# Kernel optimization log

Hardware: AMD Instinct MI355X
Metric: run time of the kernel (lower is better)

## Reference

```python
import jax, jax.numpy as jnp
import numpy as np

N, E, G = 100000, 1600000, 64
IN, H, OUT = 128, 64, 16  # hidden/2 = 32
SLOPE = 0.01


def setup_inputs() -> dict:
    key = jax.random.key(0)
    ks = jax.random.split(key, 7)
    features = jax.random.normal(ks[0], (N, IN), dtype=jnp.float32)
    src = jax.random.randint(ks[1], (E,), 0, N)
    dst = jax.random.randint(ks[2], (E,), 0, N)
    graph_ids = jnp.sort(jax.random.randint(ks[3], (N,), 0, G))
    # kaiming-uniform-ish fan_in init, bias=False everywhere
    W1 = jax.random.uniform(ks[4], (IN, H), jnp.float32, -1.0, 1.0) * np.sqrt(3.0 / IN)
    W2 = jax.random.uniform(ks[5], (H, H // 2), jnp.float32, -1.0, 1.0) * np.sqrt(3.0 / H)
    Wc = jax.random.uniform(ks[6], (H // 2, OUT), jnp.float32, -1.0, 1.0) * np.sqrt(3.0 / (H // 2))
    return {"features": features, "src": src, "dst": dst, "graph_ids": graph_ids,
            "W1": W1, "W2": W2, "Wc": Wc}


def _graph_conv(x, W, src, dst, n):
    # DGL GraphConv, norm='both', bias=False:
    # out = D_in^{-1/2} A (D_out^{-1/2} x) W   (degrees clamped to >= 1)
    ones = jnp.ones(src.shape[0], dtype=x.dtype)
    outdeg = jnp.clip(jax.ops.segment_sum(ones, src, num_segments=n), 1.0)
    indeg = jnp.clip(jax.ops.segment_sum(ones, dst, num_segments=n), 1.0)
    h = (x * jax.lax.rsqrt(outdeg)[:, None]) @ W  # project first (in_dim > out_dim)
    m = jax.ops.segment_sum(h[src], dst, num_segments=n)  # sparse aggregation
    return m * jax.lax.rsqrt(indeg)[:, None]


def reference(features, src, dst, graph_ids, W1, W2, Wc):
    h = jax.nn.leaky_relu(_graph_conv(features, W1, src, dst, N), SLOPE)
    h = jax.nn.leaky_relu(_graph_conv(h, W2, src, dst, N), SLOPE)
    # dropout is identity at inference
    sums = jax.ops.segment_sum(h, graph_ids, num_segments=G)
    cnts = jnp.clip(jax.ops.segment_sum(jnp.ones((N,), h.dtype), graph_ids, num_segments=G), 1.0)
    mean = sums / cnts[:, None]  # dgl.mean_nodes
    return mean @ Wc  # [G, OUT]
```

## Files before the change

kernel.cpp:

```cpp
#include <hip/hip_runtime.h>

#define NN 100000
#define NE 1600000
#define NG 64
#define D_IN 128
#define D_H 64
#define D_H2 32
#define D_OUT 16
#define SLOPE 0.01f
#define REC 48

#define BSH 9
#define NBK 196
#define NCB 250
#define CHE (NE / NCB)
#define CNT_M (2 * NBK * NCB)
#define CNT_R 98048

typedef _Float16 half2v __attribute__((ext_vector_type(2)));
typedef _Float16 h8 __attribute__((ext_vector_type(8)));
typedef float f32x4 __attribute__((ext_vector_type(4)));

__global__ __launch_bounds__(256) void p1_count(const int* __restrict__ src,
                                                const int* __restrict__ dst,
                                                int* __restrict__ cnt) {
  __shared__ int hD[NBK], hS[NBK];
  int b = blockIdx.x, t = threadIdx.x;
  if (b == 0 && t < CNT_R - CNT_M) cnt[CNT_M + t] = 0;
  for (int i = t; i < NBK; i += 256) { hD[i] = 0; hS[i] = 0; }
  __syncthreads();
  const int4* s4 = (const int4*)(src + b * CHE);
  const int4* d4 = (const int4*)(dst + b * CHE);
  for (int i = t; i < CHE / 4; i += 256) {
    int4 s = s4[i], d = d4[i];
    atomicAdd(&hD[d.x >> BSH], 1); atomicAdd(&hD[d.y >> BSH], 1);
    atomicAdd(&hD[d.z >> BSH], 1); atomicAdd(&hD[d.w >> BSH], 1);
    atomicAdd(&hS[s.x >> BSH], 1); atomicAdd(&hS[s.y >> BSH], 1);
    atomicAdd(&hS[s.z >> BSH], 1); atomicAdd(&hS[s.w >> BSH], 1);
  }
  __syncthreads();
  for (int i = t; i < NBK; i += 256) {
    cnt[i * NCB + b] = hD[i];
    cnt[(NBK + i) * NCB + b] = hS[i];
  }
}

__global__ __launch_bounds__(256) void s1_reduce(const int* __restrict__ cnt,
                                                 int* __restrict__ part) {
  __shared__ int red[256];
  int b = blockIdx.x, t = threadIdx.x;
  red[t] = cnt[b * 256 + t];
  __syncthreads();
  for (int off = 128; off > 0; off >>= 1) {
    if (t < off) red[t] += red[t + off];
    __syncthreads();
  }
  if (t == 0) part[b] = red[0];
}

__global__ __launch_bounds__(512) void s2_scan(int* __restrict__ part) {
  __shared__ int a[512], b2[512];
  int t = threadIdx.x;
  const int M = CNT_R / 256;
  int v = (t < M) ? part[t] : 0;
  a[t] = v;
  __syncthreads();
  int* cur = a; int* nxt = b2;
  for (int off = 1; off < 512; off <<= 1) {
    int x = cur[t];
    if (t >= off) x += cur[t - off];
    nxt[t] = x;
    __syncthreads();
    int* tmp = cur; cur = nxt; nxt = tmp;
  }
  if (t < M) part[t] = cur[t] - v;
}

__global__ __launch_bounds__(256) void s3_apply(int* __restrict__ cnt,
                                                const int* __restrict__ part) {
  __shared__ int wsum[4];
  int b = blockIdx.x, t = threadIdx.x;
  int gid = b * 256 + t;
  int v0 = cnt[gid];
  int lane = t & 63, w = t >> 6;
  int v = v0;
  for (int off = 1; off < 64; off <<= 1) {
    int u = __shfl_up(v, off);
    if (lane >= off) v += u;
  }
  if (lane == 63) wsum[w] = v;
  __syncthreads();
  int woff = 0;
  for (int i = 0; i < w; ++i) woff += wsum[i];
  cnt[gid] = part[b] + woff + (v - v0);
}

__global__ __launch_bounds__(256) void p2_scatter(const int* __restrict__ src,
                                                  const int* __restrict__ dst,
                                                  const int* __restrict__ cnt,
                                                  unsigned* __restrict__ pk,
                                                  unsigned short* __restrict__ srcs16) {
  __shared__ int cD[NBK], cS[NBK];
  int b = blockIdx.x, t = threadIdx.x;
  for (int i = t; i < NBK; i += 256) {
    cD[i] = cnt[i * NCB + b];
    cS[i] = cnt[(NBK + i) * NCB + b] - NE;
  }
  __syncthreads();
  const int4* s4 = (const int4*)(src + b * CHE);
  const int4* d4 = (const int4*)(dst + b * CHE);
  for (int i = t; i < CHE / 4; i += 256) {
    int4 s = s4[i], d = d4[i];
#pragma unroll
    for (int j = 0; j < 4; ++j) {
      int ss = (j == 0) ? s.x : (j == 1) ? s.y : (j == 2) ? s.z : s.w;
      int dd = (j == 0) ? d.x : (j == 1) ? d.y : (j == 2) ? d.z : d.w;
      int pd = atomicAdd(&cD[dd >> BSH], 1);
      pk[pd] = ((unsigned)(dd & 511) << 17) | (unsigned)ss;
      int ps = atomicAdd(&cS[ss >> BSH], 1);
      srcs16[ps] = (unsigned short)(ss & 511);
    }
  }
}

__global__ __launch_bounds__(256) void p3_build(const unsigned* __restrict__ pk,
                                                const unsigned short* __restrict__ srcs16,
                                                const int* __restrict__ cnt,
                                                int* __restrict__ adj,
                                                int* __restrict__ indeg,
                                                int* __restrict__ outdeg) {
  __shared__ int hh[512];
  int bb = blockIdx.x, t = threadIdx.x;
  for (int i = t; i < 512; i += 256) hh[i] = 0;
  __syncthreads();
  if (bb < NBK) {
    int k = bb;
    int n0 = k << BSH;
    int lo = cnt[k * NCB];
    int hi = cnt[(k + 1) * NCB];
    for (int i = lo + t; i < hi; i += 256) {
      unsigned v = pk[i];
      int local = v >> 17;
      int pos = atomicAdd(&hh[local], 1);
      if (pos < REC) adj[(size_t)(n0 + local) * REC + pos] = (int)(v & 0x1FFFF);
    }
    __syncthreads();
    for (int i = t; i < 512; i += 256) {
      int n = n0 + i;
      if (n < NN) {
        int dg = hh[i];
        indeg[n] = dg;
        int d = min(dg, REC);
        int dr = min((d + 15) & ~15, REC);
        for (int j = d; j < dr; ++j) adj[(size_t)n * REC + j] = NN;
      }
    }
  } else {
    int k = bb - NBK;
    int lo = cnt[(NBK + k) * NCB] - NE;
    int hi = ((k == NBK - 1) ? 2 * NE : cnt[(NBK + k + 1) * NCB]) - NE;
    for (int i = lo + t; i < hi; i += 256) atomicAdd(&hh[srcs16[i]], 1);
    __syncthreads();
    int n0 = k << BSH;
    for (int i = t; i < 512; i += 256) {
      int n = n0 + i;
      if (n < NN) outdeg[n] = hh[i];
    }
  }
}

__global__ __launch_bounds__(256) void k_mm1f(const float* __restrict__ X,
                                              const float* __restrict__ W,
                                              const int* __restrict__ odeg,
                                              _Float16* __restrict__ Y) {
  __shared__ _Float16 Wt[64][136];
  int t = threadIdx.x;
  if (blockIdx.x == 0 && t < 64) Y[(size_t)NN * 64 + t] = (_Float16)0.f;
  for (int i = t; i < 128 * 64; i += 256) {
    int k = i >> 6, f = i & 63;
    Wt[f][k] = (_Float16)W[i];
  }
  __syncthreads();
  int lane = t & 63, w = t >> 6;
  int m = lane & 15, q = lane >> 4;
  h8 bf[4][4];
#pragma unroll
  for (int kc = 0; kc < 4; ++kc)
#pragma unroll
    for (int nt = 0; nt < 4; ++nt)
      bf[kc][nt] = *(const h8*)&Wt[nt * 16 + m][kc * 32 + q * 8];

  for (int tile = blockIdx.x * 4 + w; tile < NN / 16; tile += gridDim.x * 4) {
    int n0 = tile * 16;
    const f32x4* Xr = (const f32x4*)(X + (size_t)(n0 + m) * 128);
    h8 af[4];
#pragma unroll
    for (int kc = 0; kc < 4; ++kc) {
      f32x4 x0 = Xr[kc * 8 + q * 2 + 0];
      f32x4 x1 = Xr[kc * 8 + q * 2 + 1];
      h8 a;
      a[0] = (_Float16)x0.x; a[1] = (_Float16)x0.y;
      a[2] = (_Float16)x0.z; a[3] = (_Float16)x0.w;
      a[4] = (_Float16)x1.x; a[5] = (_Float16)x1.y;
      a[6] = (_Float16)x1.z; a[7] = (_Float16)x1.w;
      af[kc] = a;
    }
    f32x4 acc[4] = {{0,0,0,0},{0,0,0,0},{0,0,0,0},{0,0,0,0}};
#pragma unroll
    for (int kc = 0; kc < 4; ++kc)
#pragma unroll
      for (int nt = 0; nt < 4; ++nt)
        acc[nt] = __builtin_amdgcn_mfma_f32_16x16x32_f16(af[kc], bf[kc][nt], acc[nt], 0, 0, 0);
#pragma unroll
    for (int reg = 0; reg < 4; ++reg) {
      int nn = n0 + q * 4 + reg;
      float sc = rsqrtf((float)max(odeg[nn], 1));
#pragma unroll
      for (int nt = 0; nt < 4; ++nt)
        Y[(size_t)nn * 64 + nt * 16 + m] = (_Float16)(acc[nt][reg] * sc);
    }
  }
}

__global__ __launch_bounds__(256) void k_mm2f(const _Float16* __restrict__ Xh,
                                              const float* __restrict__ W,
                                              const int* __restrict__ odeg,
                                              _Float16* __restrict__ Y) {
  __shared__ _Float16 Wt[32][72];
  int t = threadIdx.x;
  if (blockIdx.x == 0 && t < 32) Y[(size_t)NN * 32 + t] = (_Float16)0.f;
  for (int i = t; i < 64 * 32; i += 256) {
    int k = i >> 5, f = i & 31;
    Wt[f][k] = (_Float16)W[i];
  }
  __syncthreads();
  int lane = t & 63, w = t >> 6;
  int m = lane & 15, q = lane >> 4;
  h8 bf[2][2];
#pragma unroll
  for (int kc = 0; kc < 2; ++kc)
#pragma unroll
    for (int nt = 0; nt < 2; ++nt)
      bf[kc][nt] = *(const h8*)&Wt[nt * 16 + m][kc * 32 + q * 8];

  for (int tile = blockIdx.x * 4 + w; tile < NN / 16; tile += gridDim.x * 4) {
    int n0 = tile * 16;
    const h8* Xr = (const h8*)(Xh + (size_t)(n0 + m) * 64);
    h8 af[2];
#pragma unroll
    for (int kc = 0; kc < 2; ++kc) af[kc] = Xr[kc * 4 + q];
    f32x4 acc[2] = {{0,0,0,0},{0,0,0,0}};
#pragma unroll
    for (int kc = 0; kc < 2; ++kc)
#pragma unroll
      for (int nt = 0; nt < 2; ++nt)
        acc[nt] = __builtin_amdgcn_mfma_f32_16x16x32_f16(af[kc], bf[kc][nt], acc[nt], 0, 0, 0);
#pragma unroll
    for (int reg = 0; reg < 4; ++reg) {
      int nn = n0 + q * 4 + reg;
      float sc = rsqrtf((float)max(odeg[nn], 1));
#pragma unroll
      for (int nt = 0; nt < 2; ++nt)
        Y[(size_t)nn * 32 + nt * 16 + m] = (_Float16)(acc[nt][reg] * sc);
    }
  }
}

__global__ __launch_bounds__(256) void k_agg64(const int* __restrict__ adj,
                                               const int* __restrict__ indeg,
                                               const half2v* __restrict__ H2,
                                               half2v* __restrict__ Y2) {
  int lane = threadIdx.x & 31;
  int node = blockIdx.x * 8 + (threadIdx.x >> 5);
  int deg = indeg[node];
  int groups = (min(deg, REC) + 15) >> 4;
  const int4* c4 = (const int4*)(adj + (size_t)node * REC);
  float sx = 0.f, sy = 0.f;
  for (int g = 0; g < groups; ++g) {
    int4 ca = c4[g * 4 + 0], cb = c4[g * 4 + 1];
    int4 cc = c4[g * 4 + 2], cd = c4[g * 4 + 3];
    half2v v0 = H2[(size_t)ca.x * 32 + lane];
    half2v v1 = H2[(size_t)ca.y * 32 + lane];
    half2v v2 = H2[(size_t)ca.z * 32 + lane];
    half2v v3 = H2[(size_t)ca.w * 32 + lane];
    half2v v4 = H2[(size_t)cb.x * 32 + lane];
    half2v v5 = H2[(size_t)cb.y * 32 + lane];
    half2v v6 = H2[(size_t)cb.z * 32 + lane];
    half2v v7 = H2[(size_t)cb.w * 32 + lane];
    half2v v8 = H2[(size_t)cc.x * 32 + lane];
    half2v v9 = H2[(size_t)cc.y * 32 + lane];
    half2v va = H2[(size_t)cc.z * 32 + lane];
    half2v vb = H2[(size_t)cc.w * 32 + lane];
    half2v vc = H2[(size_t)cd.x * 32 + lane];
    half2v vd = H2[(size_t)cd.y * 32 + lane];
    half2v ve = H2[(size_t)cd.z * 32 + lane];
    half2v vf = H2[(size_t)cd.w * 32 + lane];
    sx += (((float)v0.x + (float)v1.x) + ((float)v2.x + (float)v3.x)) +
          (((float)v4.x + (float)v5.x) + ((float)v6.x + (float)v7.x)) +
          (((float)v8.x + (float)v9.x) + ((float)va.x + (float)vb.x)) +
          (((float)vc.x + (float)vd.x) + ((float)ve.x + (float)vf.x));
    sy += (((float)v0.y + (float)v1.y) + ((float)v2.y + (float)v3.y)) +
          (((float)v4.y + (float)v5.y) + ((float)v6.y + (float)v7.y)) +
          (((float)v8.y + (float)v9.y) + ((float)va.y + (float)vb.y)) +
          (((float)vc.y + (float)vd.y) + ((float)ve.y + (float)vf.y));
  }
  float sc = rsqrtf((float)max(deg, 1));
  sx *= sc; sy *= sc;
  half2v o = {(_Float16)((sx > 0.f) ? sx : SLOPE * sx),
              (_Float16)((sy > 0.f) ? sy : SLOPE * sy)};
  Y2[(size_t)node * 32 + lane] = o;
}

__global__ __launch_bounds__(256) void k_agg32(const int* __restrict__ adj,
                                               const int* __restrict__ indeg,
                                               const half2v* __restrict__ H2,
                                               half2v* __restrict__ Y2) {
  int lane = threadIdx.x & 15;
  int node = blockIdx.x * 16 + (threadIdx.x >> 4);
  int deg = indeg[node];
  int groups = (min(deg, REC) + 15) >> 4;
  const int4* c4 = (const int4*)(adj + (size_t)node * REC);
  float sx = 0.f, sy = 0.f;
  for (int g = 0; g < groups; ++g) {
    int4 ca = c4[g * 4 + 0], cb = c4[g * 4 + 1];
    int4 cc = c4[g * 4 + 2], cd = c4[g * 4 + 3];
    half2v v0 = H2[(size_t)ca.x * 16 + lane];
    half2v v1 = H2[(size_t)ca.y * 16 + lane];
    half2v v2 = H2[(size_t)ca.z * 16 + lane];
    half2v v3 = H2[(size_t)ca.w * 16 + lane];
    half2v v4 = H2[(size_t)cb.x * 16 + lane];
    half2v v5 = H2[(size_t)cb.y * 16 + lane];
    half2v v6 = H2[(size_t)cb.z * 16 + lane];
    half2v v7 = H2[(size_t)cb.w * 16 + lane];
    half2v v8 = H2[(size_t)cc.x * 16 + lane];
    half2v v9 = H2[(size_t)cc.y * 16 + lane];
    half2v va = H2[(size_t)cc.z * 16 + lane];
    half2v vb = H2[(size_t)cc.w * 16 + lane];
    half2v vc = H2[(size_t)cd.x * 16 + lane];
    half2v vd = H2[(size_t)cd.y * 16 + lane];
    half2v ve = H2[(size_t)cd.z * 16 + lane];
    half2v vf = H2[(size_t)cd.w * 16 + lane];
    sx += (((float)v0.x + (float)v1.x) + ((float)v2.x + (float)v3.x)) +
          (((float)v4.x + (float)v5.x) + ((float)v6.x + (float)v7.x)) +
          (((float)v8.x + (float)v9.x) + ((float)va.x + (float)vb.x)) +
          (((float)vc.x + (float)vd.x) + ((float)ve.x + (float)vf.x));
    sy += (((float)v0.y + (float)v1.y) + ((float)v2.y + (float)v3.y)) +
          (((float)v4.y + (float)v5.y) + ((float)v6.y + (float)v7.y)) +
          (((float)v8.y + (float)v9.y) + ((float)va.y + (float)vb.y)) +
          (((float)vc.y + (float)vd.y) + ((float)ve.y + (float)vf.y));
  }
  float sc = rsqrtf((float)max(deg, 1));
  sx *= sc; sy *= sc;
  half2v o = {(_Float16)((sx > 0.f) ? sx : SLOPE * sx),
              (_Float16)((sy > 0.f) ? sy : SLOPE * sy)};
  Y2[(size_t)node * 16 + lane] = o;
}

__global__ void k_bounds(const int* __restrict__ gid, int* __restrict__ bounds) {
  int n = blockIdx.x * 256 + threadIdx.x;
  if (n < NN) {
    int g = gid[n];
    int gp = (n == 0) ? -1 : gid[n - 1];
    for (int j = gp + 1; j <= g; ++j) bounds[j] = n;
    if (n == NN - 1)
      for (int j = g + 1; j <= NG; ++j) bounds[j] = NN;
  }
}

__global__ __launch_bounds__(256) void k_poolout(const half2v* __restrict__ H2,
                                                 const int* __restrict__ bounds,
                                                 const float* __restrict__ Wc,
                                                 float* __restrict__ out) {
  __shared__ float red[16][33];
  __shared__ float mean[D_H2];
  int g = blockIdx.x, t = threadIdx.x;
  int start = bounds[g], end = bounds[g + 1];
  int c2 = t & 15, r = t >> 4;
  float sx = 0.f, sy = 0.f;
  for (int n = start + r; n < end; n += 16) {
    half2v v = H2[(size_t)n * 16 + c2];
    sx += (float)v.x;
    sy += (float)v.y;
  }
  red[r][c2 * 2] = sx;
  red[r][c2 * 2 + 1] = sy;
  __syncthreads();
  if (r < 8) { red[r][c2 * 2] += red[r + 8][c2 * 2]; red[r][c2 * 2 + 1] += red[r + 8][c2 * 2 + 1]; }
  __syncthreads();
  if (r < 4) { red[r][c2 * 2] += red[r + 4][c2 * 2]; red[r][c2 * 2 + 1] += red[r + 4][c2 * 2 + 1]; }
  __syncthreads();
  if (r < 2) { red[r][c2 * 2] += red[r + 2][c2 * 2]; red[r][c2 * 2 + 1] += red[r + 2][c2 * 2 + 1]; }
  __syncthreads();
  if (r == 0) {
    float inv = 1.0f / (float)max(end - start, 1);
    mean[c2 * 2] = (red[0][c2 * 2] + red[1][c2 * 2]) * inv;
    mean[c2 * 2 + 1] = (red[0][c2 * 2 + 1] + red[1][c2 * 2 + 1]) * inv;
  }
  __syncthreads();
  if (t < D_OUT) {
    float acc = 0.f;
#pragma unroll
    for (int cc = 0; cc < D_H2; ++cc) acc += mean[cc] * Wc[cc * D_OUT + t];
    out[g * D_OUT + t] = acc;
  }
}

extern "C" void kernel_launch(void* const* d_in, const int* in_sizes, int n_in,
                              void* d_out, int out_size, void* d_ws, size_t ws_size,
                              hipStream_t stream) {
  const float* X  = (const float*)d_in[0];
  const int*   src = (const int*)d_in[1];
  const int*   dst = (const int*)d_in[2];
  const int*   gid = (const int*)d_in[3];
  const float* W1 = (const float*)d_in[4];
  const float* W2 = (const float*)d_in[5];
  const float* Wc = (const float*)d_in[6];
  float* out = (float*)d_out;

  char* p = (char*)d_ws;
  auto alloc = [&](size_t bytes) {
    char* q = p;
    p += (bytes + 255) & ~(size_t)255;
    return q;
  };
  int*            outdeg = (int*)alloc(NN * 4);
  int*            indeg  = (int*)alloc(NN * 4);
  int*            bounds = (int*)alloc((NG + 1) * 4);
  int*            cnt    = (int*)alloc((CNT_R + 256) * 4);
  int*            part   = (int*)alloc((CNT_R / 256) * 4);
  unsigned*       pk     = (unsigned*)alloc((size_t)NE * 4);
  unsigned short* srcs16 = (unsigned short*)alloc((size_t)NE * 2);
  int*            adj    = (int*)alloc((size_t)NN * REC * 4);
  _Float16*       bufA   = (_Float16*)alloc((size_t)(NN + 1) * 64 * 2);
  _Float16*       bufB   = (_Float16*)alloc((size_t)(NN + 1) * 64 * 2);

  p1_count<<<NCB, 256, 0, stream>>>(src, dst, cnt);
  s1_reduce<<<CNT_R / 256, 256, 0, stream>>>(cnt, part);
  s2_scan<<<1, 512, 0, stream>>>(part);
  s3_apply<<<CNT_R / 256, 256, 0, stream>>>(cnt, part);
  p2_scatter<<<NCB, 256, 0, stream>>>(src, dst, cnt, pk, srcs16);
  p3_build<<<2 * NBK, 256, 0, stream>>>(pk, srcs16, cnt, adj, indeg, outdeg);
  k_bounds<<<(NN + 255) / 256, 256, 0, stream>>>(gid, bounds);

  k_mm1f<<<1563, 256, 0, stream>>>(X, W1, outdeg, bufA);
  k_agg64<<<NN / 8, 256, 0, stream>>>(adj, indeg, (const half2v*)bufA, (half2v*)bufB);

  k_mm2f<<<1563, 256, 0, stream>>>(bufB, W2, outdeg, bufA);
  k_agg32<<<NN / 16, 256, 0, stream>>>(adj, indeg, (const half2v*)bufA, (half2v*)bufB);

  k_poolout<<<NG, 256, 0, stream>>>((const half2v*)bufB, bounds, Wc, out);
}
```

Measured before the change: 245.0 us.

## Fuse layer-1 aggregation with layer-2 matmul, vectorize gathers, drop scan/bounds kernels

Merges the 64-wide aggregation and the W2 projection into one kernel: it gathers neighbor rows with 16-byte loads into shared memory, then runs MFMA on 32-node tiles, so the intermediate never goes through global memory. The 32-wide aggregation now uses h8 vector loads with 4 lanes per node. The single-block scan is replaced by having each apply block reduce its prefix directly, and the graph-bounds kernel is replaced by a binary search inside pooling. Fewer launches and wider gathers are traded for redundant prefix sums and idle waves in the MFMA stage.

New measurement: 240.3 us. About the same (-1.9%).

```diff
diff --git a/kernel.cpp b/kernel.cpp
--- a/kernel.cpp
+++ b/kernel.cpp
@@ -58,28 +58,20 @@
   if (t == 0) part[b] = red[0];
 }
 
-__global__ __launch_bounds__(512) void s2_scan(int* __restrict__ part) {
-  __shared__ int a[512], b2[512];
-  int t = threadIdx.x;
-  const int M = CNT_R / 256;
-  int v = (t < M) ? part[t] : 0;
-  a[t] = v;
-  __syncthreads();
-  int* cur = a; int* nxt = b2;
-  for (int off = 1; off < 512; off <<= 1) {
-    int x = cur[t];
-    if (t >= off) x += cur[t - off];
-    nxt[t] = x;
-    __syncthreads();
-    int* tmp = cur; cur = nxt; nxt = tmp;
-  }
-  if (t < M) part[t] = cur[t] - v;
-}
-
-__global__ __launch_bounds__(256) void s3_apply(int* __restrict__ cnt,
-                                                const int* __restrict__ part) {
+__global__ __launch_bounds__(256) void s3_apply2(int* __restrict__ cnt,
+                                                 const int* __restrict__ part) {
+  __shared__ int red[256];
   __shared__ int wsum[4];
   int b = blockIdx.x, t = threadIdx.x;
+  int s = 0;
+  for (int i = t; i < b; i += 256) s += part[i];
+  red[t] = s;
+  __syncthreads();
+  for (int off = 128; off > 0; off >>= 1) {
+    if (t < off) red[t] += red[t + off];
+    __syncthreads();
+  }
+  int base = red[0];
   int gid = b * 256 + t;
   int v0 = cnt[gid];
   int lane = t & 63, w = t >> 6;
@@ -92,7 +84,7 @@
   __syncthreads();
   int woff = 0;
   for (int i = 0; i < w; ++i) woff += wsum[i];
-  cnt[gid] = part[b] + woff + (v - v0);
+  cnt[gid] = base + woff + (v - v0);
 }
 
 __global__ __launch_bounds__(256) void p2_scatter(const int* __restrict__ src,
@@ -222,10 +214,13 @@
   }
 }
 
-__global__ __launch_bounds__(256) void k_mm2f(const _Float16* __restrict__ Xh,
-                                              const float* __restrict__ W,
-                                              const int* __restrict__ odeg,
-                                              _Float16* __restrict__ Y) {
+__global__ __launch_bounds__(256) void k_aggmm2(const int* __restrict__ adj,
+                                                const int* __restrict__ indeg,
+                                                const int* __restrict__ odeg,
+                                                const h8* __restrict__ H8,
+                                                const float* __restrict__ W,
+                                                _Float16* __restrict__ Y) {
+  __shared__ _Float16 Ht[32][72];
   __shared__ _Float16 Wt[32][72];
   int t = threadIdx.x;
   if (blockIdx.x == 0 && t < 32) Y[(size_t)NN * 32 + t] = (_Float16)0.f;
@@ -233,148 +228,156 @@
     int k = i >> 5, f = i & 31;
     Wt[f][k] = (_Float16)W[i];
   }
-  __syncthreads();
-  int lane = t & 63, w = t >> 6;
-  int m = lane & 15, q = lane >> 4;
-  h8 bf[2][2];
-#pragma unroll
-  for (int kc = 0; kc < 2; ++kc)
-#pragma unroll
-    for (int nt = 0; nt < 2; ++nt)
-      bf[kc][nt] = *(const h8*)&Wt[nt * 16 + m][kc * 32 + q * 8];
-
-  for (int tile = blockIdx.x * 4 + w; tile < NN / 16; tile += gridDim.x * 4) {
-    int n0 = tile * 16;
-    const h8* Xr = (const h8*)(Xh + (size_t)(n0 + m) * 64);
-    h8 af[2];
-#pragma unroll
-    for (int kc = 0; kc < 2; ++kc) af[kc] = Xr[kc * 4 + q];
-    f32x4 acc[2] = {{0,0,0,0},{0,0,0,0}};
-#pragma unroll
-    for (int kc = 0; kc < 2; ++kc)
-#pragma unroll
-      for (int nt = 0; nt < 2; ++nt)
-        acc[nt] = __builtin_amdgcn_mfma_f32_16x16x32_f16(af[kc], bf[kc][nt], acc[nt], 0, 0, 0);
-#pragma unroll
-    for (int reg = 0; reg < 4; ++reg) {
-      int nn = n0 + q * 4 + reg;
-      float sc = rsqrtf((float)max(odeg[nn], 1));
-#pragma unroll
-      for (int nt = 0; nt < 2; ++nt)
-        Y[(size_t)nn * 32 + nt * 16 + m] = (_Float16)(acc[nt][reg] * sc);
-    }
-  }
-}
-
-__global__ __launch_bounds__(256) void k_agg64(const int* __restrict__ adj,
-                                               const int* __restrict__ indeg,
-                                               const half2v* __restrict__ H2,
-                                               half2v* __restrict__ Y2) {
-  int lane = threadIdx.x & 31;
-  int node = blockIdx.x * 8 + (threadIdx.x >> 5);
+  int l8 = t & 7;
+  int nd = t >> 3;
+  int node = blockIdx.x * 32 + nd;
   int deg = indeg[node];
   int groups = (min(deg, REC) + 15) >> 4;
   const int4* c4 = (const int4*)(adj + (size_t)node * REC);
-  float sx = 0.f, sy = 0.f;
+  float acc[8] = {0.f, 0.f, 0.f, 0.f, 0.f, 0.f, 0.f, 0.f};
   for (int g = 0; g < groups; ++g) {
     int4 ca = c4[g * 4 + 0], cb = c4[g * 4 + 1];
+    {
+      h8 v0 = H8[(size_t)ca.x * 8 + l8];
+      h8 v1 = H8[(size_t)ca.y * 8 + l8];
+      h8 v2 = H8[(size_t)ca.z * 8 + l8];
+      h8 v3 = H8[(size_t)ca.w * 8 + l8];
+      h8 v4 = H8[(size_t)cb.x * 8 + l8];
+      h8 v5 = H8[(size_t)cb.y * 8 + l8];
+      h8 v6 = H8[(size_t)cb.z * 8 + l8];
+      h8 v7 = H8[(size_t)cb.w * 8 + l8];
+#pragma unroll
+      for (int j = 0; j < 8; ++j)
+        acc[j] += (((float)v0[j] + (float)v1[j]) + ((float)v2[j] + (float)v3[j])) +
+                  (((float)v4[j] + (float)v5[j]) + ((float)v6[j] + (float)v7[j]));
+    }
     int4 cc = c4[g * 4 + 2], cd = c4[g * 4 + 3];
-    half2v v0 = H2[(size_t)ca.x * 32 + lane];
-    half2v v1 = H2[(size_t)ca.y * 32 + lane];
-    half2v v2 = H2[(size_t)ca.z * 32 + lane];
-    half2v v3 = H2[(size_t)ca.w * 32 + lane];
-    half2v v4 = H2[(size_t)cb.x * 32 + lane];
-    half2v v5 = H2[(size_t)cb.y * 32 + lane];
-    half2v v6 = H2[(size_t)cb.z * 32 + lane];
-    half2v v7 = H2[(size_t)cb.w * 32 + lane];
-    half2v v8 = H2[(size_t)cc.x * 32 + lane];
-    half2v v9 = H2[(size_t)cc.y * 32 + lane];
-    half2v va = H2[(size_t)cc.z * 32 + lane];
-    half2v vb = H2[(size_t)cc.w * 32 + lane];
-    half2v vc = H2[(size_t)cd.x * 32 + lane];
-    half2v vd = H2[(size_t)cd.y * 32 + lane];
-    half2v ve = H2[(size_t)cd.z * 32 + lane];
-    half2v vf = H2[(size_t)cd.w * 32 + lane];
-    sx += (((float)v0.x + (float)v1.x) + ((float)v2.x + (float)v3.x)) +
-          (((float)v4.x + (float)v5.x) + ((float)v6.x + (float)v7.x)) +
-          (((float)v8.x + (float)v9.x) + ((float)va.x + (float)vb.x)) +
-          (((float)vc.x + (float)vd.x) + ((float)ve.x + (float)vf.x));
-    sy += (((float)v0.y + (float)v1.y) + ((float)v2.y + (float)v3.y)) +
-          (((float)v4.y + (float)v5.y) + ((float)v6.y + (float)v7.y)) +
-          (((float)v8.y + (float)v9.y) + ((float)va.y + (float)vb.y)) +
-          (((float)vc.y + (float)vd.y) + ((float)ve.y + (float)vf.y));
+    {
+      h8 v0 = H8[(size_t)cc.x * 8 + l8];
+      h8 v1 = H8[(size_t)cc.y * 8 + l8];
+      h8 v2 = H8[(size_t)cc.z * 8 + l8];
+      h8 v3 = H8[(size_t)cc.w * 8 + l8];
+      h8 v4 = H8[(size_t)cd.x * 8 + l8];
+      h8 v5 = H8[(size_t)cd.y * 8 + l8];
+      h8 v6 = H8[(size_t)cd.z * 8 + l8];
+      h8 v7 = H8[(size_t)cd.w * 8 + l8];
+#pragma unroll
+      for (int j = 0; j < 8; ++j)
+        acc[j] += (((float)v0[j] + (float)v1[j]) + ((float)v2[j] + (float)v3[j])) +
+                  (((float)v4[j] + (float)v5[j]) + ((float)v6[j] + (float)v7[j]));
+    }
   }
   float sc = rsqrtf((float)max(deg, 1));
-  sx *= sc; sy *= sc;
-  half2v o = {(_Float16)((sx > 0.f) ? sx : SLOPE * sx),
-              (_Float16)((sy > 0.f) ? sy : SLOPE * sy)};
-  Y2[(size_t)node * 32 + lane] = o;
-}
-
-__global__ __launch_bounds__(256) void k_agg32(const int* __restrict__ adj,
-                                               const int* __restrict__ indeg,
-                                               const half2v* __restrict__ H2,
-                                               half2v* __restrict__ Y2) {
-  int lane = threadIdx.x & 15;
-  int node = blockIdx.x * 16 + (threadIdx.x >> 4);
+  h8 hv;
+#pragma unroll
+  for (int j = 0; j < 8; ++j) {
+    float x = acc[j] * sc;
+    hv[j] = (_Float16)((x > 0.f) ? x : SLOPE * x);
+  }
+  *(h8*)&Ht[nd][l8 * 8] = hv;
+  __syncthreads();
+  int lane = t & 63, w = t >> 6;
+  if (w < 2) {
+    int m = lane & 15, q = lane >> 4;
+    h8 bf[2][2];
+#pragma unroll
+    for (int kc = 0; kc < 2; ++kc)
+#pragma unroll
+      for (int nt = 0; nt < 2; ++nt)
+        bf[kc][nt] = *(const h8*)&Wt[nt * 16 + m][kc * 32 + q * 8];
+    h8 af[2];
+#pragma unroll
+    for (int kc = 0; kc < 2; ++kc)
+      af[kc] = *(const h8*)&Ht[w * 16 + m][kc * 32 + q * 8];
+    f32x4 acc2[2] = {{0, 0, 0, 0}, {0, 0, 0, 0}};
+#pragma unroll
+    for (int kc = 0; kc < 2; ++kc)
+#pragma unroll
+      for (int nt = 0; nt < 2; ++nt)
+        acc2[nt] = __builtin_amdgcn_mfma_f32_16x16x32_f16(af[kc], bf[kc][nt], acc2[nt], 0, 0, 0);
+#pragma unroll
+    for (int reg = 0; reg < 4; ++reg) {
+      int nn = blockIdx.x * 32 + w * 16 + q * 4 + reg;
+      float sco = rsqrtf((float)max(odeg[nn], 1));
+#pragma unroll
+      for (int nt = 0; nt < 2; ++nt)
+        Y[(size_t)nn * 32 + nt * 16 + m] = (_Float16)(acc2[nt][reg] * sco);
+    }
+  }
+}
+
+__global__ __launch_bounds__(256) void k_agg32v(const int* __restrict__ adj,
+                                                const int* __restrict__ indeg,
+                                                const h8* __restrict__ H8,
+                                                h8* __restrict__ Y8) {
+  int l4 = threadIdx.x & 3;
+  int node = blockIdx.x * 64 + (threadIdx.x >> 2);
+  if (node >= NN) return;
   int deg = indeg[node];
   int groups = (min(deg, REC) + 15) >> 4;
   const int4* c4 = (const int4*)(adj + (size_t)node * REC);
-  float sx = 0.f, sy = 0.f;
+  float acc[8] = {0.f, 0.f, 0.f, 0.f, 0.f, 0.f, 0.f, 0.f};
   for (int g = 0; g < groups; ++g) {
     int4 ca = c4[g * 4 + 0], cb = c4[g * 4 + 1];
+    {
+      h8 v0 = H8[(size_t)ca.x * 4 + l4];
+      h8 v1 = H8[(size_t)ca.y * 4 + l4];
+      h8 v2 = H8[(size_t)ca.z * 4 + l4];
+      h8 v3 = H8[(size_t)ca.w * 4 + l4];
+      h8 v4 = H8[(size_t)cb.x * 4 + l4];
+      h8 v5 = H8[(size_t)cb.y * 4 + l4];
+      h8 v6 = H8[(size_t)cb.z * 4 + l4];
+      h8 v7 = H8[(size_t)cb.w * 4 + l4];
+#pragma unroll
+      for (int j = 0; j < 8; ++j)
+        acc[j] += (((float)v0[j] + (float)v1[j]) + ((float)v2[j] + (float)v3[j])) +
+                  (((float)v4[j] + (float)v5[j]) + ((float)v6[j] + (float)v7[j]));
+    }
     int4 cc = c4[g * 4 + 2], cd = c4[g * 4 + 3];
-    half2v v0 = H2[(size_t)ca.x * 16 + lane];
-    half2v v1 = H2[(size_t)ca.y * 16 + lane];
-    half2v v2 = H2[(size_t)ca.z * 16 + lane];
-    half2v v3 = H2[(size_t)ca.w * 16 + lane];
-    half2v v4 = H2[(size_t)cb.x * 16 + lane];
-    half2v v5 = H2[(size_t)cb.y * 16 + lane];
-    half2v v6 = H2[(size_t)cb.z * 16 + lane];
-    half2v v7 = H2[(size_t)cb.w * 16 + lane];
-    half2v v8 = H2[(size_t)cc.x * 16 + lane];
-    half2v v9 = H2[(size_t)cc.y * 16 + lane];
-    half2v va = H2[(size_t)cc.z * 16 + lane];
-    half2v vb = H2[(size_t)cc.w * 16 + lane];
-    half2v vc = H2[(size_t)cd.x * 16 + lane];
-    half2v vd = H2[(size_t)cd.y * 16 + lane];
-    half2v ve = H2[(size_t)cd.z * 16 + lane];
-    half2v vf = H2[(size_t)cd.w * 16 + lane];
-    sx += (((float)v0.x + (float)v1.x) + ((float)v2.x + (float)v3.x)) +
-          (((float)v4.x + (float)v5.x) + ((float)v6.x + (float)v7.x)) +
-          (((float)v8.x + (float)v9.x) + ((float)va.x + (float)vb.x)) +
-          (((float)vc.x + (float)vd.x) + ((float)ve.x + (float)vf.x));
-    sy += (((float)v0.y + (float)v1.y) + ((float)v2.y + (float)v3.y)) +
-          (((float)v4.y + (float)v5.y) + ((float)v6.y + (float)v7.y)) +
-          (((float)v8.y + (float)v9.y) + ((float)va.y + (float)vb.y)) +
-          (((float)vc.y + (float)vd.y) + ((float)ve.y + (float)vf.y));
+    {
+      h8 v0 = H8[(size_t)cc.x * 4 + l4];
+      h8 v1 = H8[(size_t)cc.y * 4 + l4];
+      h8 v2 = H8[(size_t)cc.z * 4 + l4];
+      h8 v3 = H8[(size_t)cc.w * 4 + l4];
+      h8 v4 = H8[(size_t)cd.x * 4 + l4];
+      h8 v5 = H8[(size_t)cd.y * 4 + l4];
+      h8 v6 = H8[(size_t)cd.z * 4 + l4];
+      h8 v7 = H8[(size_t)cd.w * 4 + l4];
+#pragma unroll
+      for (int j = 0; j < 8; ++j)
+        acc[j] += (((float)v0[j] + (float)v1[j]) + ((float)v2[j] + (float)v3[j])) +
+                  (((float)v4[j] + (float)v5[j]) + ((float)v6[j] + (float)v7[j]));
+    }
   }
   float sc = rsqrtf((float)max(deg, 1));
-  sx *= sc; sy *= sc;
-  half2v o = {(_Float16)((sx > 0.f) ? sx : SLOPE * sx),
-              (_Float16)((sy > 0.f) ? sy : SLOPE * sy)};
-  Y2[(size_t)node * 16 + lane] = o;
-}
-
-__global__ void k_bounds(const int* __restrict__ gid, int* __restrict__ bounds) {
-  int n = blockIdx.x * 256 + threadIdx.x;
-  if (n < NN) {
-    int g = gid[n];
-    int gp = (n == 0) ? -1 : gid[n - 1];
-    for (int j = gp + 1; j <= g; ++j) bounds[j] = n;
-    if (n == NN - 1)
-      for (int j = g + 1; j <= NG; ++j) bounds[j] = NN;
-  }
+  h8 o;
+#pragma unroll
+  for (int j = 0; j < 8; ++j) {
+    float x = acc[j] * sc;
+    o[j] = (_Float16)((x > 0.f) ? x : SLOPE * x);
+  }
+  Y8[(size_t)node * 4 + l4] = o;
 }
 
 __global__ __launch_bounds__(256) void k_poolout(const half2v* __restrict__ H2,
-                                                 const int* __restrict__ bounds,
+                                                 const int* __restrict__ gid,
                                                  const float* __restrict__ Wc,
                                                  float* __restrict__ out) {
   __shared__ float red[16][33];
   __shared__ float mean[D_H2];
+  __shared__ int sb[2];
   int g = blockIdx.x, t = threadIdx.x;
-  int start = bounds[g], end = bounds[g + 1];
+  if (t < 2) {
+    int target = g + t;
+    int lo = 0, hi = NN;
+    while (lo < hi) {
+      int mid = (lo + hi) >> 1;
+      if (gid[mid] < target) lo = mid + 1; else hi = mid;
+    }
+    sb[t] = lo;
+  }
+  __syncthreads();
+  int start = sb[0], end = sb[1];
   int c2 = t & 15, r = t >> 4;
   float sx = 0.f, sy = 0.f;
   for (int n = start + r; n < end; n += 16) {
@@ -425,28 +428,24 @@
   };
   int*            outdeg = (int*)alloc(NN * 4);
   int*            indeg  = (int*)alloc(NN * 4);
-  int*            bounds = (int*)alloc((NG + 1) * 4);
   int*            cnt    = (int*)alloc((CNT_R + 256) * 4);
   int*            part   = (int*)alloc((CNT_R / 256) * 4);
   unsigned*       pk     = (unsigned*)alloc((size_t)NE * 4);
   unsigned short* srcs16 = (unsigned short*)alloc((size_t)NE * 2);
   int*            adj    = (int*)alloc((size_t)NN * REC * 4);
   _Float16*       bufA   = (_Float16*)alloc((size_t)(NN + 1) * 64 * 2);
-  _Float16*       bufB   = (_Float16*)alloc((size_t)(NN + 1) * 64 * 2);
+  _Float16*       bufB   = (_Float16*)alloc((size_t)(NN + 1) * 32 * 2);
+  _Float16*       bufC   = (_Float16*)alloc((size_t)(NN + 1) * 32 * 2);
 
   p1_count<<<NCB, 256, 0, stream>>>(src, dst, cnt);
   s1_reduce<<<CNT_R / 256, 256, 0, stream>>>(cnt, part);
-  s2_scan<<<1, 512, 0, stream>>>(part);
-  s3_apply<<<CNT_R / 256, 256, 0, stream>>>(cnt, part);
+  s3_apply2<<<CNT_R / 256, 256, 0, stream>>>(cnt, part);
   p2_scatter<<<NCB, 256, 0, stream>>>(src, dst, cnt, pk, srcs16);
   p3_build<<<2 * NBK, 256, 0, stream>>>(pk, srcs16, cnt, adj, indeg, outdeg);
-  k_bounds<<<(NN + 255) / 256, 256, 0, stream>>>(gid, bounds);
 
   k_mm1f<<<1563, 256, 0, stream>>>(X, W1, outdeg, bufA);
-  k_agg64<<<NN / 8, 256, 0, stream>>>(adj, indeg, (const half2v*)bufA, (half2v*)bufB);
-
-  k_mm2f<<<1563, 256, 0, stream>>>(bufB, W2, outdeg, bufA);
-  k_agg32<<<NN / 16, 256, 0, stream>>>(adj, indeg, (const half2v*)bufA, (half2v*)bufB);
-
-  k_poolout<<<NG, 256, 0, stream>>>((const half2v*)bufB, bounds, Wc, out);
-}
+  k_aggmm2<<<NN / 32, 256, 0, stream>>>(adj, indeg, outdeg, (const h8*)bufA, W2, bufC);
+  k_agg32v<<<(NN + 63) / 64, 256, 0, stream>>>(adj, indeg, (const h8*)bufC, (h8*)bufB);
+
+  k_poolout<<<NG, 256, 0, stream>>>((const half2v*)bufB, gid, Wc, out);
+}
```
